# Optimization experiments

Hardware: AMD Instinct MI355X
Metric: run time of the kernel (lower is better)

The kernel has to match this reference:

```python
import jax, jax.numpy as jnp
import numpy as np

N = 100000      # nodes
DEG = 16        # in-degree per node -> E = 1.6M edges
F = 16          # data.x feature dim (19 total - 3 pos dims)
P = 3           # pos dim
H = 64          # hidden_dim
R = 8           # num_regions
C = 8           # num_classes


def _xavier(k, shp):
    lim = np.sqrt(6.0 / (shp[0] + shp[1])).astype(np.float32)
    return jax.random.uniform(k, shp, jnp.float32, -lim, lim)


def setup_inputs() -> dict:
    key = jax.random.key(0)
    ks = jax.random.split(key, 16)
    x = jax.random.normal(ks[0], (N, F), jnp.float32)
    pos = jax.random.uniform(ks[1], (N, P), jnp.float32)
    # every node is a target exactly DEG times so scatter-max is fully covered
    src = jax.random.randint(ks[2], (N * DEG,), 0, N, jnp.int32)
    tgt = jnp.repeat(jnp.arange(N, dtype=jnp.int32), DEG)
    edge_index = jnp.stack([src, tgt])
    # ---- CPU quotient-graph construction (mirrors sklearn KMeans + 3-NN) ----
    pos_np = np.asarray(pos)
    rng = np.random.RandomState(0)
    centers = pos_np[rng.choice(N, R, replace=False)].copy()
    for _ in range(10):  # Lloyd iterations
        d = ((pos_np[:, None, :] - centers[None, :, :]) ** 2).sum(-1)
        labels = d.argmin(1)
        for i in range(R):
            m = labels == i
            if m.any():
                centers[i] = pos_np[m].mean(0)
    cd = ((centers[:, None, :] - centers[None, :, :]) ** 2).sum(-1)
    nn_idx = np.argsort(cd, axis=1)[:, :3]
    conn = []
    for i in range(R):
        for j in nn_idx[i, 1:]:
            conn.append([i, j]); conn.append([j, i])
    quotient_edge_index = jnp.asarray(np.array(conn).T, jnp.int32)
    cluster_labels = jnp.asarray(labels, jnp.int32)
    # ---- parameters (xavier_uniform weights, zero bias) ----
    out = dict(x=x, pos=pos, edge_index=edge_index,
               cluster_labels=cluster_labels,
               quotient_edge_index=quotient_edge_index)
    in_dims = [2 * (F + P), 2 * H, 2 * H, 2 * H]
    for i in range(4):
        out[f"conv{i+1}_W1"] = _xavier(ks[3 + 2 * i], (in_dims[i], H))
        out[f"conv{i+1}_b1"] = jnp.zeros((H,), jnp.float32)
        out[f"conv{i+1}_W2"] = _xavier(ks[4 + 2 * i], (H, H))
        out[f"conv{i+1}_b2"] = jnp.zeros((H,), jnp.float32)
    out["lin_W"] = _xavier(ks[11], (H, C))
    out["lin_b"] = jnp.zeros((C,), jnp.float32)
    return out


def _edge_conv(x, edge_index, W1, b1, W2, b2, num_nodes):
    src, tgt = edge_index[0], edge_index[1]
    x_i = x[tgt]                         # [E, d] target (center)
    x_j = x[src]                         # [E, d] source (neighbor)
    m = jnp.concatenate([x_i, x_j - x_i], axis=1)   # [E, 2d]
    m = jax.nn.relu(m @ W1 + b1) @ W2 + b2          # [E, H]
    agg = jax.ops.segment_max(m, tgt, num_segments=num_nodes)
    # nodes with no incoming edges -> 0 (torch_scatter semantics)
    return jnp.where(jnp.isfinite(agg), agg, 0.0)


def reference(x, pos, edge_index, cluster_labels, quotient_edge_index,
              conv1_W1, conv1_b1, conv1_W2, conv1_b2,
              conv2_W1, conv2_b1, conv2_W2, conv2_b2,
              conv3_W1, conv3_b1, conv3_W2, conv3_b2,
              conv4_W1, conv4_b1, conv4_W2, conv4_b2,
              lin_W, lin_b):
    h = jnp.concatenate([x, pos], axis=1)                       # [N, 19]
    h = jax.nn.relu(_edge_conv(h, edge_index, conv1_W1, conv1_b1, conv1_W2, conv1_b2, N))
    h = jax.nn.relu(_edge_conv(h, edge_index, conv2_W1, conv2_b1, conv2_W2, conv2_b2, N))
    # quotient graph: per-region mean of node features
    sums = jax.ops.segment_sum(h, cluster_labels, num_segments=R)        # [R, H]
    cnt = jax.ops.segment_sum(jnp.ones((h.shape[0], 1), h.dtype), cluster_labels, num_segments=R)
    qx = jnp.where(cnt > 0, sums / jnp.maximum(cnt, 1.0), 0.0)           # [R, H]
    qx = jax.nn.relu(_edge_conv(qx, quotient_edge_index, conv3_W1, conv3_b1, conv3_W2, conv3_b2, R))
    qx = jax.nn.relu(_edge_conv(qx, quotient_edge_index, conv4_W1, conv4_b1, conv4_W2, conv4_b2, R))
    graph_emb = qx.sum(axis=0, keepdims=True)                    # global_add_pool -> [1, H]
    return graph_emb @ lin_W + lin_b                             # [1, C]
```

## Files before the change

### kernel.cpp

```cpp
#include <hip/hip_runtime.h>
#include <hip/hip_fp16.h>

typedef float fv4 __attribute__((ext_vector_type(4)));
using hf8   = __attribute__((ext_vector_type(8))) _Float16;
using f32x4 = __attribute__((ext_vector_type(4))) float;
using u32x4 = __attribute__((ext_vector_type(4))) unsigned;

#define HDIM 64

__device__ __forceinline__ unsigned short f16r(float f) {
    return __half_as_ushort(__float2half(f));
}
__device__ __forceinline__ float hs2f(unsigned short s) {
    return __half2float(__ushort_as_half(s));
}
__device__ __forceinline__ unsigned addrelu2(unsigned ua, unsigned va) {
    unsigned s, r;
    asm("v_pk_add_f16 %0, %1, %2" : "=v"(s) : "v"(ua), "v"(va));
    asm("v_pk_max_f16 %0, %1, 0" : "=v"(r) : "v"(s));
    return r;
}

__global__ void pre1_kernel(
    const float* __restrict__ x, const float* __restrict__ pos,
    const float* __restrict__ W1, const float* __restrict__ b1,
    unsigned short* __restrict__ U, unsigned short* __restrict__ V, int N,
    int mainBlocks,
    const float* __restrict__ W2a, const float* __restrict__ W2b,
    const float* __restrict__ W1c,
    unsigned short* __restrict__ hiA, unsigned short* __restrict__ loA,
    unsigned short* __restrict__ hiB, unsigned short* __restrict__ loB,
    unsigned short* __restrict__ wph, unsigned short* __restrict__ wpl,
    int* __restrict__ qzero)
{
    if ((int)blockIdx.x >= mainBlocks) {
        int idx = (blockIdx.x - mainBlocks) * 256 + threadIdx.x;
        if (idx < 520) qzero[idx] = 0;
        if (idx < 4096) {
            int j = idx >> 6, c = idx & 63;
            float w = W2a[idx];
            unsigned short h = f16r(w);
            unsigned short l = f16r(w - hs2f(h));
            hiA[c * 64 + j] = h; loA[c * 64 + j] = l;
            w = W2b[idx];
            h = f16r(w);
            l = f16r(w - hs2f(h));
            hiB[c * 64 + j] = h; loB[c * 64 + j] = l;
        }
        if (idx < 8192) {
            int d = idx & 63, cp = idx >> 6;
            float w = (cp < 64) ? (W1c[d * 64 + cp] - W1c[(d + 64) * 64 + cp])
                                : W1c[(d + 64) * 64 + (cp - 64)];
            unsigned short h = f16r(w);
            unsigned short l = f16r(w - hs2f(h));
            wph[cp * 64 + d] = h;
            wpl[cp * 64 + d] = l;
        }
        return;
    }

    int lane = threadIdx.x & 63;
    int gw   = (blockIdx.x * blockDim.x + threadIdx.x) >> 6;
    int tw   = (mainBlocks * blockDim.x) >> 6;

    float wd[19], wb[19];
#pragma unroll
    for (int d = 0; d < 19; ++d) {
        float a = W1[d * HDIM + lane];
        float b = W1[(d + 19) * HDIM + lane];
        wd[d] = a - b;
        wb[d] = b;
    }
    float bb = b1[lane];

    for (int n = gw; n < N; n += tw) {
        float su = 0.f, sv = 0.f;
#pragma unroll
        for (int d4 = 0; d4 < 4; ++d4) {
            fv4 h4 = *(const fv4*)&x[(size_t)n * 16 + 4 * d4];
#pragma unroll
            for (int k = 0; k < 4; ++k) {
                su += h4[k] * wd[4 * d4 + k];
                sv += h4[k] * wb[4 * d4 + k];
            }
        }
#pragma unroll
        for (int d = 0; d < 3; ++d) {
            float h = pos[(size_t)n * 3 + d];
            su += h * wd[16 + d];
            sv += h * wb[16 + d];
        }
        U[(size_t)n * HDIM + lane] = f16r(su + bb);
        V[(size_t)n * HDIM + lane] = f16r(sv);
    }
}

__global__ __launch_bounds__(256, 2) void pre_mfma_kernel(
    const unsigned short* __restrict__ h,
    const unsigned short* __restrict__ Whi,
    const unsigned short* __restrict__ Wlo,
    const float* __restrict__ b1,
    unsigned short* __restrict__ U, unsigned short* __restrict__ V, int nTiles)
{
    int lane = threadIdx.x & 63;
    int quad = lane >> 4;
    int m    = lane & 15;
    int gw   = (blockIdx.x * blockDim.x + threadIdx.x) >> 6;
    int tw   = (gridDim.x * blockDim.x) >> 6;

    hf8 Bh[8][2], Bl[8][2];
#pragma unroll
    for (int nt = 0; nt < 8; ++nt)
#pragma unroll
        for (int ks = 0; ks < 2; ++ks) {
            int off = (nt * 16 + m) * 64 + ks * 32 + quad * 8;
            Bh[nt][ks] = *(const hf8*)&Whi[off];
            Bl[nt][ks] = *(const hf8*)&Wlo[off];
        }
    float bias[4];
#pragma unroll
    for (int nt = 0; nt < 4; ++nt) bias[nt] = b1[nt * 16 + m];

    for (int t = gw; t < nTiles; t += tw) {
        int base = t * 16;
        hf8 A[2];
#pragma unroll
        for (int ks = 0; ks < 2; ++ks)
            A[ks] = *(const hf8*)&h[(size_t)(base + m) * HDIM + ks * 32 + quad * 8];

        f32x4 acc[8] = {{0,0,0,0},{0,0,0,0},{0,0,0,0},{0,0,0,0},
                        {0,0,0,0},{0,0,0,0},{0,0,0,0},{0,0,0,0}};
#pragma unroll
        for (int ks = 0; ks < 2; ++ks)
#pragma unroll
            for (int nt = 0; nt < 8; ++nt) {
                acc[nt] = __builtin_amdgcn_mfma_f32_16x16x32_f16(A[ks], Bl[nt][ks], acc[nt], 0, 0, 0);
                acc[nt] = __builtin_amdgcn_mfma_f32_16x16x32_f16(A[ks], Bh[nt][ks], acc[nt], 0, 0, 0);
            }

#pragma unroll
        for (int nt = 0; nt < 8; ++nt) {
            float bv = (nt < 4) ? bias[nt] : 0.f;
            unsigned short* __restrict__ dst = (nt < 4) ? U : V;
            int cc = (nt & 3) * 16 + m;
#pragma unroll
            for (int r = 0; r < 4; ++r) {
                int node = base + quad * 4 + r;
                dst[(size_t)node * HDIM + cc] = f16r(acc[nt][r] + bv);
            }
        }
    }
}

#define FOLD_HALF(V0, V1, OFF)                                                     \
    _Pragma("unroll")                                                              \
    for (int mt = 0; mt < 4; ++mt) {                                               \
        int urow = wave * 8 + (OFF) + mt;                                          \
        u32x4 u0 = *(const u32x4*)((const char*)Ush + urow * 128 + quad * 16);     \
        u32x4 u1 = *(const u32x4*)((const char*)Ush + urow * 128 + 64 + quad * 16);\
        u32x4 a0, a1;                                                              \
        _Pragma("unroll")                                                          \
        for (int p = 0; p < 4; ++p) {                                              \
            a0[p] = addrelu2(u0[p], V0[mt][p]);                                    \
            a1[p] = addrelu2(u1[p], V1[mt][p]);                                    \
        }                                                                          \
        hf8 A0 = __builtin_bit_cast(hf8, a0);                                      \
        hf8 A1 = __builtin_bit_cast(hf8, a1);                                      \
        f32x4 acc[4] = {{0,0,0,0},{0,0,0,0},{0,0,0,0},{0,0,0,0}};                  \
        _Pragma("unroll")                                                          \
        for (int nt = 0; nt < 4; ++nt) {                                           \
            int bb  = nt * 2048 + m * 128 + quad * 16;                             \
            int bs0 = bb ^ ((m & 7) << 4);                                         \
            int bs1 = (bb + 64) ^ ((m & 7) << 4);                                  \
            hf8 Bh0 = *(const hf8*)((const char*)Wsh + bs0);                       \
            hf8 Bl0 = *(const hf8*)((const char*)Wsh + 8192 + bs0);                \
            hf8 Bh1 = *(const hf8*)((const char*)Wsh + bs1);                       \
            hf8 Bl1 = *(const hf8*)((const char*)Wsh + 8192 + bs1);                \
            acc[nt] = __builtin_amdgcn_mfma_f32_16x16x32_f16(A0, Bl0, acc[nt], 0, 0, 0); \
            acc[nt] = __builtin_amdgcn_mfma_f32_16x16x32_f16(A0, Bh0, acc[nt], 0, 0, 0); \
            acc[nt] = __builtin_amdgcn_mfma_f32_16x16x32_f16(A1, Bl1, acc[nt], 0, 0, 0); \
            acc[nt] = __builtin_amdgcn_mfma_f32_16x16x32_f16(A1, Bh1, acc[nt], 0, 0, 0); \
        }                                                                          \
        float mx[4];                                                               \
        _Pragma("unroll")                                                          \
        for (int nt = 0; nt < 4; ++nt)                                             \
            mx[nt] = fmaxf(fmaxf(acc[nt][0], acc[nt][1]), fmaxf(acc[nt][2], acc[nt][3])); \
        _Pragma("unroll")                                                          \
        for (int nt = 0; nt < 4; ++nt) {                                           \
            mx[nt] = fmaxf(mx[nt], __shfl_xor(mx[nt], 16));                        \
            mx[nt] = fmaxf(mx[nt], __shfl_xor(mx[nt], 32));                        \
        }                                                                          \
        float val = (quad == 0) ? mx[0] : (quad == 1) ? mx[1] : (quad == 2) ? mx[2] : mx[3]; \
        out[(size_t)(nb + (OFF) + mt) * HDIM + lane] = f16r(fmaxf(val + b2v, 0.f));\
    }

__global__ __launch_bounds__(256, 3) void edge_mfma_kernel(
    const unsigned short* __restrict__ U, const unsigned short* __restrict__ V,
    const int* __restrict__ src,
    const unsigned short* __restrict__ Whi, const unsigned short* __restrict__ Wlo,
    const float* __restrict__ b2, unsigned short* __restrict__ out)
{
    __shared__ __align__(16) unsigned short Wsh[8192];
    __shared__ __align__(16) unsigned short Ush[2048];

    int tid  = threadIdx.x;
    int wave = tid >> 6;
    int lane = tid & 63;
    int quad = lane >> 4;
    int m    = lane & 15;

    int nbB = blockIdx.x * 32;
    int nb  = nbB + wave * 8;

#pragma unroll
    for (int it = 0; it < 4; ++it) {
        int chunk = it * 256 + tid;
        int reg   = it >> 1;
        int b     = (chunk & 511) * 16;
        int bs    = b ^ (((b >> 7) & 7) << 4);
        const unsigned short* sp = reg ? Wlo : Whi;
        u32x4 d = *(const u32x4*)((const char*)sp + b);
        *(u32x4*)((char*)Wsh + reg * 8192 + bs) = d;
    }
    *(u32x4*)((char*)Ush + tid * 16) =
        *(const u32x4*)((const char*)(U + (size_t)nbB * HDIM) + tid * 16);

    int  srcA = src[(size_t)nb * 16 + lane];
    int  srcB = src[(size_t)(nb + 4) * 16 + lane];
    float b2v = b2[lane];

    __syncthreads();

    u32x4 vA0[4], vA1[4], vB0[4], vB1[4];
#pragma unroll
    for (int mt = 0; mt < 4; ++mt) {
        int s_ = __shfl(srcA, mt * 16 + m);
        const u32x4* vp = (const u32x4*)(V + (size_t)s_ * HDIM + quad * 8);
        vA0[mt] = vp[0]; vA1[mt] = vp[4];
    }
#pragma unroll
    for (int mt = 0; mt < 4; ++mt) {
        int s_ = __shfl(srcB, mt * 16 + m);
        const u32x4* vp = (const u32x4*)(V + (size_t)s_ * HDIM + quad * 8);
        vB0[mt] = vp[0]; vB1[mt] = vp[4];
    }

    FOLD_HALF(vA0, vA1, 0)
    FOLD_HALF(vB0, vB1, 4)
}

__global__ void region_mean_kernel(const unsigned short* __restrict__ h,
                                   const int* __restrict__ labels,
                                   float* __restrict__ qsums, int* __restrict__ qcnt, int N)
{
    __shared__ float ls[8 * 64];
    __shared__ int   lc[8];
    int tid  = threadIdx.x;
    int lane = tid & 63;
    int gw   = (blockIdx.x * blockDim.x + tid) >> 6;
    int tw   = (gridDim.x * blockDim.x) >> 6;

    float acc[8] = {0, 0, 0, 0, 0, 0, 0, 0};
    int   cnt[8] = {0, 0, 0, 0, 0, 0, 0, 0};

    for (int n = gw; n < N; n += tw) {
        int lbl = labels[n];
        float val = hs2f(h[(size_t)n * HDIM + lane]);
#pragma unroll
        for (int r = 0; r < 8; ++r) {
            acc[r] += (lbl == r) ? val : 0.f;
            cnt[r] += (lbl == r) ? 1 : 0;
        }
    }

    if (tid < 8) lc[tid] = 0;
    for (int idx = tid; idx < 512; idx += 256) ls[idx] = 0.f;
    __syncthreads();
#pragma unroll
    for (int r = 0; r < 8; ++r) atomicAdd(&ls[r * 64 + lane], acc[r]);
    if (lane == 0)
#pragma unroll
        for (int r = 0; r < 8; ++r) atomicAdd(&lc[r], cnt[r]);
    __syncthreads();
    for (int idx = tid; idx < 512; idx += 256) atomicAdd(&qsums[idx], ls[idx]);
    if (tid < 8) atomicAdd(&qcnt[tid], lc[tid]);
}

#define EQ_MAX 64
__global__ void tail_kernel(const float* __restrict__ qsums, const int* __restrict__ qcnt,
                            const int* __restrict__ qei, int Eq,
                            const float* __restrict__ W31, const float* __restrict__ b31,
                            const float* __restrict__ W32, const float* __restrict__ b32,
                            const float* __restrict__ W41, const float* __restrict__ b41,
                            const float* __restrict__ W42, const float* __restrict__ b42,
                            const float* __restrict__ linW, const float* __restrict__ linb,
                            float* __restrict__ out)
{
    __shared__ float qx[512], uu[512], vv[512];
    __shared__ float hr[EQ_MAX * 64], me[EQ_MAX * 64];
    __shared__ __align__(16) float W2s[64 * 64];
    __shared__ int   qes[EQ_MAX], qet[EQ_MAX];
    __shared__ float emb[64];

    int tid = threadIdx.x;
    if (Eq > EQ_MAX) Eq = EQ_MAX;

    if (tid < Eq) { qes[tid] = qei[tid]; qet[tid] = qei[Eq + tid]; }
    for (int idx = tid; idx < 512; idx += 256) {
        int r = idx >> 6;
        int cc = qcnt[r];
        qx[idx] = (cc > 0) ? qsums[idx] / (float)cc : 0.f;
    }
    __syncthreads();

    for (int layer = 0; layer < 2; ++layer) {
        const float* W1p = layer ? W41 : W31;
        const float* b1p = layer ? b41 : b31;
        const float* W2p = layer ? W42 : W32;
        const float* b2p = layer ? b42 : b32;

        for (int idx = tid * 4; idx < 4096; idx += 1024)
            *(fv4*)&W2s[idx] = *(const fv4*)&W2p[idx];

        for (int idx = tid; idx < 512; idx += 256) {
            int t = idx >> 6, c = idx & 63;
            float su = 0.f, sv = 0.f;
#pragma unroll 8
            for (int d = 0; d < 64; ++d) {
                float hv = qx[t * 64 + d];
                float a = W1p[d * 64 + c];
                float b = W1p[(d + 64) * 64 + c];
                su += hv * (a - b);
                sv += hv * b;
            }
            uu[idx] = su + b1p[c];
            vv[idx] = sv;
        }
        __syncthreads();

        for (int idx = tid; idx < Eq * 64; idx += 256) {
            int e = idx >> 6, c = idx & 63;
            hr[idx] = fmaxf(uu[qet[e] * 64 + c] + vv[qes[e] * 64 + c], 0.f);
        }
        __syncthreads();

        {
            int c = tid & 63, e0 = tid >> 6;
            for (int e = e0; e < Eq; e += 4) {
                float acc = 0.f;
#pragma unroll 8
                for (int j = 0; j < 64; ++j)
                    acc += hr[e * 64 + j] * W2s[j * 64 + c];
                me[e * 64 + c] = acc;
            }
        }
        __syncthreads();

        for (int idx = tid; idx < 512; idx += 256) {
            int t = idx >> 6, c = idx & 63;
            float a = -INFINITY;
            for (int e = 0; e < Eq; ++e)
                if (qet[e] == t) a = fmaxf(a, me[e * 64 + c]);
            float vout = (a == -INFINITY) ? 0.f : (a + b2p[c]);
            qx[idx] = fmaxf(vout, 0.f);
        }
        __syncthreads();
    }

    if (tid < 64) {
        float s = 0.f;
        for (int r = 0; r < 8; ++r) s += qx[r * 64 + tid];
        emb[tid] = s;
    }
    __syncthreads();
    if (tid < 8) {
        float o = linb[tid];
        for (int c = 0; c < 64; ++c) o += emb[c] * linW[c * 8 + tid];
        out[tid] = o;
    }
}

extern "C" void kernel_launch(void* const* d_in, const int* in_sizes, int n_in,
                              void* d_out, int out_size, void* d_ws, size_t ws_size,
                              hipStream_t stream)
{
    const float* x    = (const float*)d_in[0];
    const float* pos  = (const float*)d_in[1];
    const int*   ei   = (const int*)d_in[2];
    const int*   lbl  = (const int*)d_in[3];
    const int*   qei  = (const int*)d_in[4];
    const float* W11 = (const float*)d_in[5];
    const float* b11 = (const float*)d_in[6];
    const float* W12 = (const float*)d_in[7];
    const float* b12 = (const float*)d_in[8];
    const float* W21 = (const float*)d_in[9];
    const float* b21 = (const float*)d_in[10];
    const float* W22 = (const float*)d_in[11];
    const float* b22 = (const float*)d_in[12];
    const float* W31 = (const float*)d_in[13];
    const float* b31 = (const float*)d_in[14];
    const float* W32 = (const float*)d_in[15];
    const float* b32 = (const float*)d_in[16];
    const float* W41 = (const float*)d_in[17];
    const float* b41 = (const float*)d_in[18];
    const float* W42 = (const float*)d_in[19];
    const float* b42 = (const float*)d_in[20];
    const float* linW = (const float*)d_in[21];
    const float* linb = (const float*)d_in[22];

    int N  = in_sizes[0] / 16;
    int Eq = in_sizes[4] / 2;
    const int* src = ei;

    size_t NH = (size_t)N * HDIM;
    unsigned short* hbf = (unsigned short*)d_ws;
    unsigned short* Ub  = hbf + NH;
    unsigned short* Vb  = Ub + NH;
    unsigned short* w2h1 = Vb + NH;
    unsigned short* w2l1 = w2h1 + 4096;
    unsigned short* w2h2 = w2l1 + 4096;
    unsigned short* w2l2 = w2h2 + 4096;
    unsigned short* wph  = w2l2 + 4096;
    unsigned short* wpl  = wph + 8192;
    float* qsums = (float*)(wpl + 8192);
    int*   qcnt  = (int*)(qsums + 512);

    int nTiles      = N / 16;
    int edgeBlocks  = N / 32;
    int mainBlocks  = 2048;

    pre1_kernel<<<mainBlocks + 32, 256, 0, stream>>>(
        x, pos, W11, b11, Ub, Vb, N, mainBlocks,
        W12, W22, W21, w2h1, w2l1, w2h2, w2l2, wph, wpl, (int*)qsums);
    edge_mfma_kernel<<<edgeBlocks, 256, 0, stream>>>(Ub, Vb, src, w2h1, w2l1, b12, hbf);
    pre_mfma_kernel<<<512, 256, 0, stream>>>(hbf, wph, wpl, b21, Ub, Vb, nTiles);
    edge_mfma_kernel<<<edgeBlocks, 256, 0, stream>>>(Ub, Vb, src, w2h2, w2l2, b22, hbf);
    region_mean_kernel<<<1024, 256, 0, stream>>>(hbf, lbl, qsums, qcnt, N);
    tail_kernel<<<1, 256, 0, stream>>>(qsums, qcnt, qei, Eq,
                                       W31, b31, W32, b32,
                                       W41, b41, W42, b42,
                                       linW, linb, (float*)d_out);
}
```

Baseline: 287.3 us.

## Fuse region-mean pooling into second edge kernel and widen edge tiles

Removes the separate region-mean kernel by accumulating per-label sums in registers inside the second edge-conv kernel, skipping the write of the final node features. Label counts move into pre1's auxiliary blocks and zeroing moves to a memset. The edge kernel now processes 16 nodes per wave with gathers interleaved between folds to overlap latency. The pre-MFMA kernel swaps operands so it can store packed 4-element f16 vectors, and its grid grows. The cost is higher register pressure and larger shared-memory use per block.

```diff
diff --git a/kernel.cpp b/kernel.cpp
--- a/kernel.cpp
+++ b/kernel.cpp
@@ -5,6 +5,7 @@
 using hf8   = __attribute__((ext_vector_type(8))) _Float16;
 using f32x4 = __attribute__((ext_vector_type(4))) float;
 using u32x4 = __attribute__((ext_vector_type(4))) unsigned;
+using u32x2 = __attribute__((ext_vector_type(2))) unsigned;
 
 #define HDIM 64
 
@@ -31,11 +32,10 @@
     unsigned short* __restrict__ hiA, unsigned short* __restrict__ loA,
     unsigned short* __restrict__ hiB, unsigned short* __restrict__ loB,
     unsigned short* __restrict__ wph, unsigned short* __restrict__ wpl,
-    int* __restrict__ qzero)
+    const int* __restrict__ labels, int* __restrict__ qcnt)
 {
     if ((int)blockIdx.x >= mainBlocks) {
         int idx = (blockIdx.x - mainBlocks) * 256 + threadIdx.x;
-        if (idx < 520) qzero[idx] = 0;
         if (idx < 4096) {
             int j = idx >> 6, c = idx & 63;
             float w = W2a[idx];
@@ -55,6 +55,21 @@
             unsigned short l = f16r(w - hs2f(h));
             wph[cp * 64 + d] = h;
             wpl[cp * 64 + d] = l;
+        }
+        {
+            __shared__ int lh[8];
+            int loc[8] = {0, 0, 0, 0, 0, 0, 0, 0};
+            for (int n = idx; n < N; n += 8192) {
+                int l = labels[n];
+#pragma unroll
+                for (int r = 0; r < 8; ++r) loc[r] += (l == r) ? 1 : 0;
+            }
+            if (threadIdx.x < 8) lh[threadIdx.x] = 0;
+            __syncthreads();
+#pragma unroll
+            for (int r = 0; r < 8; ++r) if (loc[r]) atomicAdd(&lh[r], loc[r]);
+            __syncthreads();
+            if (threadIdx.x < 8) atomicAdd(&qcnt[threadIdx.x], lh[threadIdx.x]);
         }
         return;
     }
@@ -117,9 +132,12 @@
             Bh[nt][ks] = *(const hf8*)&Whi[off];
             Bl[nt][ks] = *(const hf8*)&Wlo[off];
         }
-    float bias[4];
-#pragma unroll
-    for (int nt = 0; nt < 4; ++nt) bias[nt] = b1[nt * 16 + m];
+    float bias[16];
+#pragma unroll
+    for (int nt = 0; nt < 4; ++nt)
+#pragma unroll
+        for (int r = 0; r < 4; ++r)
+            bias[nt * 4 + r] = b1[nt * 16 + quad * 4 + r];
 
     for (int t = gw; t < nTiles; t += tw) {
         int base = t * 16;
@@ -134,28 +152,38 @@
         for (int ks = 0; ks < 2; ++ks)
 #pragma unroll
             for (int nt = 0; nt < 8; ++nt) {
-                acc[nt] = __builtin_amdgcn_mfma_f32_16x16x32_f16(A[ks], Bl[nt][ks], acc[nt], 0, 0, 0);
-                acc[nt] = __builtin_amdgcn_mfma_f32_16x16x32_f16(A[ks], Bh[nt][ks], acc[nt], 0, 0, 0);
+                acc[nt] = __builtin_amdgcn_mfma_f32_16x16x32_f16(Bl[nt][ks], A[ks], acc[nt], 0, 0, 0);
+                acc[nt] = __builtin_amdgcn_mfma_f32_16x16x32_f16(Bh[nt][ks], A[ks], acc[nt], 0, 0, 0);
             }
 
 #pragma unroll
         for (int nt = 0; nt < 8; ++nt) {
-            float bv = (nt < 4) ? bias[nt] : 0.f;
             unsigned short* __restrict__ dst = (nt < 4) ? U : V;
-            int cc = (nt & 3) * 16 + m;
-#pragma unroll
-            for (int r = 0; r < 4; ++r) {
-                int node = base + quad * 4 + r;
-                dst[(size_t)node * HDIM + cc] = f16r(acc[nt][r] + bv);
-            }
-        }
-    }
-}
-
-#define FOLD_HALF(V0, V1, OFF)                                                     \
+            int c0 = (nt & 3) * 16 + quad * 4;
+            float a0 = acc[nt][0] + ((nt < 4) ? bias[nt * 4 + 0] : 0.f);
+            float a1 = acc[nt][1] + ((nt < 4) ? bias[nt * 4 + 1] : 0.f);
+            float a2 = acc[nt][2] + ((nt < 4) ? bias[nt * 4 + 2] : 0.f);
+            float a3 = acc[nt][3] + ((nt < 4) ? bias[nt * 4 + 3] : 0.f);
+            u32x2 pk;
+            pk[0] = (unsigned)f16r(a0) | ((unsigned)f16r(a1) << 16);
+            pk[1] = (unsigned)f16r(a2) | ((unsigned)f16r(a3) << 16);
+            *(u32x2*)&dst[(size_t)(base + m) * HDIM + c0] = pk;
+        }
+    }
+}
+
+#define EDGE_ISSUE(SRCR, V0, V1)                                             \
+    _Pragma("unroll")                                                        \
+    for (int mt = 0; mt < 4; ++mt) {                                         \
+        int s_ = __shfl(SRCR, mt * 16 + m);                                  \
+        const u32x4* vp = (const u32x4*)(V + (size_t)s_ * HDIM + quad * 8);  \
+        V0[mt] = vp[0]; V1[mt] = vp[4];                                      \
+    }
+
+#define EDGE_FOLD(V0, V1, OFF)                                                     \
     _Pragma("unroll")                                                              \
     for (int mt = 0; mt < 4; ++mt) {                                               \
-        int urow = wave * 8 + (OFF) + mt;                                          \
+        int urow = wave * 16 + (OFF) + mt;                                         \
         u32x4 u0 = *(const u32x4*)((const char*)Ush + urow * 128 + quad * 16);     \
         u32x4 u1 = *(const u32x4*)((const char*)Ush + urow * 128 + 64 + quad * 16);\
         u32x4 a0, a1;                                                              \
@@ -191,17 +219,26 @@
             mx[nt] = fmaxf(mx[nt], __shfl_xor(mx[nt], 32));                        \
         }                                                                          \
         float val = (quad == 0) ? mx[0] : (quad == 1) ? mx[1] : (quad == 2) ? mx[2] : mx[3]; \
-        out[(size_t)(nb + (OFF) + mt) * HDIM + lane] = f16r(fmaxf(val + b2v, 0.f));\
-    }
-
+        float hv = fmaxf(val + b2v, 0.f);                                          \
+        if constexpr (POOL) {                                                      \
+            int lbl = labels[nb + (OFF) + mt];                                     \
+            _Pragma("unroll")                                                      \
+            for (int r = 0; r < 8; ++r) pacc[r] += (lbl == r) ? hv : 0.f;          \
+        } else {                                                                   \
+            out[(size_t)(nb + (OFF) + mt) * HDIM + lane] = f16r(hv);               \
+        }                                                                          \
+    }
+
+template<int POOL>
 __global__ __launch_bounds__(256, 3) void edge_mfma_kernel(
     const unsigned short* __restrict__ U, const unsigned short* __restrict__ V,
     const int* __restrict__ src,
     const unsigned short* __restrict__ Whi, const unsigned short* __restrict__ Wlo,
-    const float* __restrict__ b2, unsigned short* __restrict__ out)
+    const float* __restrict__ b2, unsigned short* __restrict__ out,
+    const int* __restrict__ labels, float* __restrict__ qsums, int N)
 {
     __shared__ __align__(16) unsigned short Wsh[8192];
-    __shared__ __align__(16) unsigned short Ush[2048];
+    __shared__ __align__(16) unsigned short Ush[4096];
 
     int tid  = threadIdx.x;
     int wave = tid >> 6;
@@ -209,8 +246,9 @@
     int quad = lane >> 4;
     int m    = lane & 15;
 
-    int nbB = blockIdx.x * 32;
-    int nb  = nbB + wave * 8;
+    int nbB = blockIdx.x * 64;
+    int nb  = nbB + wave * 16;
+    bool act = nb < N;
 
 #pragma unroll
     for (int it = 0; it < 4; ++it) {
@@ -222,68 +260,48 @@
         u32x4 d = *(const u32x4*)((const char*)sp + b);
         *(u32x4*)((char*)Wsh + reg * 8192 + bs) = d;
     }
-    *(u32x4*)((char*)Ush + tid * 16) =
-        *(const u32x4*)((const char*)(U + (size_t)nbB * HDIM) + tid * 16);
-
-    int  srcA = src[(size_t)nb * 16 + lane];
-    int  srcB = src[(size_t)(nb + 4) * 16 + lane];
+#pragma unroll
+    for (int it = 0; it < 2; ++it) {
+        int ofs = (it * 256 + tid) * 16;
+        *(u32x4*)((char*)Ush + ofs) =
+            *(const u32x4*)((const char*)(U + (size_t)nbB * HDIM) + ofs);
+    }
+
+    int srcA = 0, srcB = 0, srcC = 0, srcD = 0;
+    if (act) {
+        srcA = src[(size_t)(nb + 0)  * 16 + lane];
+        srcB = src[(size_t)(nb + 4)  * 16 + lane];
+        srcC = src[(size_t)(nb + 8)  * 16 + lane];
+        srcD = src[(size_t)(nb + 12) * 16 + lane];
+    }
     float b2v = b2[lane];
+    float pacc[8] = {0, 0, 0, 0, 0, 0, 0, 0};
 
     __syncthreads();
 
-    u32x4 vA0[4], vA1[4], vB0[4], vB1[4];
-#pragma unroll
-    for (int mt = 0; mt < 4; ++mt) {
-        int s_ = __shfl(srcA, mt * 16 + m);
-        const u32x4* vp = (const u32x4*)(V + (size_t)s_ * HDIM + quad * 8);
-        vA0[mt] = vp[0]; vA1[mt] = vp[4];
-    }
-#pragma unroll
-    for (int mt = 0; mt < 4; ++mt) {
-        int s_ = __shfl(srcB, mt * 16 + m);
-        const u32x4* vp = (const u32x4*)(V + (size_t)s_ * HDIM + quad * 8);
-        vB0[mt] = vp[0]; vB1[mt] = vp[4];
-    }
-
-    FOLD_HALF(vA0, vA1, 0)
-    FOLD_HALF(vB0, vB1, 4)
-}
-
-__global__ void region_mean_kernel(const unsigned short* __restrict__ h,
-                                   const int* __restrict__ labels,
-                                   float* __restrict__ qsums, int* __restrict__ qcnt, int N)
-{
-    __shared__ float ls[8 * 64];
-    __shared__ int   lc[8];
-    int tid  = threadIdx.x;
-    int lane = tid & 63;
-    int gw   = (blockIdx.x * blockDim.x + tid) >> 6;
-    int tw   = (gridDim.x * blockDim.x) >> 6;
-
-    float acc[8] = {0, 0, 0, 0, 0, 0, 0, 0};
-    int   cnt[8] = {0, 0, 0, 0, 0, 0, 0, 0};
-
-    for (int n = gw; n < N; n += tw) {
-        int lbl = labels[n];
-        float val = hs2f(h[(size_t)n * HDIM + lane]);
-#pragma unroll
-        for (int r = 0; r < 8; ++r) {
-            acc[r] += (lbl == r) ? val : 0.f;
-            cnt[r] += (lbl == r) ? 1 : 0;
-        }
-    }
-
-    if (tid < 8) lc[tid] = 0;
-    for (int idx = tid; idx < 512; idx += 256) ls[idx] = 0.f;
-    __syncthreads();
-#pragma unroll
-    for (int r = 0; r < 8; ++r) atomicAdd(&ls[r * 64 + lane], acc[r]);
-    if (lane == 0)
-#pragma unroll
-        for (int r = 0; r < 8; ++r) atomicAdd(&lc[r], cnt[r]);
-    __syncthreads();
-    for (int idx = tid; idx < 512; idx += 256) atomicAdd(&qsums[idx], ls[idx]);
-    if (tid < 8) atomicAdd(&qcnt[tid], lc[tid]);
+    if (act) {
+        u32x4 vA0[4], vA1[4], vB0[4], vB1[4];
+        u32x4 vC0[4], vC1[4], vD0[4], vD1[4];
+        EDGE_ISSUE(srcA, vA0, vA1)
+        EDGE_ISSUE(srcB, vB0, vB1)
+        EDGE_FOLD(vA0, vA1, 0)
+        EDGE_ISSUE(srcC, vC0, vC1)
+        EDGE_FOLD(vB0, vB1, 4)
+        EDGE_ISSUE(srcD, vD0, vD1)
+        EDGE_FOLD(vC0, vC1, 8)
+        EDGE_FOLD(vD0, vD1, 12)
+    }
+
+    if constexpr (POOL) {
+        float* ls = (float*)Ush;
+        __syncthreads();
+        for (int idx = tid; idx < 512; idx += 256) ls[idx] = 0.f;
+        __syncthreads();
+#pragma unroll
+        for (int r = 0; r < 8; ++r) atomicAdd(&ls[r * 64 + lane], pacc[r]);
+        __syncthreads();
+        for (int idx = tid; idx < 512; idx += 256) atomicAdd(&qsums[idx], ls[idx]);
+    }
 }
 
 #define EQ_MAX 64
@@ -425,17 +443,20 @@
     float* qsums = (float*)(wpl + 8192);
     int*   qcnt  = (int*)(qsums + 512);
 
+    (void)hipMemsetAsync(qsums, 0, 512 * sizeof(float) + 8 * sizeof(int), stream);
+
     int nTiles      = N / 16;
-    int edgeBlocks  = N / 32;
+    int edgeBlocks  = (N + 63) / 64;
     int mainBlocks  = 2048;
 
     pre1_kernel<<<mainBlocks + 32, 256, 0, stream>>>(
         x, pos, W11, b11, Ub, Vb, N, mainBlocks,
-        W12, W22, W21, w2h1, w2l1, w2h2, w2l2, wph, wpl, (int*)qsums);
-    edge_mfma_kernel<<<edgeBlocks, 256, 0, stream>>>(Ub, Vb, src, w2h1, w2l1, b12, hbf);
-    pre_mfma_kernel<<<512, 256, 0, stream>>>(hbf, wph, wpl, b21, Ub, Vb, nTiles);
-    edge_mfma_kernel<<<edgeBlocks, 256, 0, stream>>>(Ub, Vb, src, w2h2, w2l2, b22, hbf);
-    region_mean_kernel<<<1024, 256, 0, stream>>>(hbf, lbl, qsums, qcnt, N);
+        W12, W22, W21, w2h1, w2l1, w2h2, w2l2, wph, wpl, lbl, qcnt);
+    edge_mfma_kernel<0><<<edgeBlocks, 256, 0, stream>>>(
+        Ub, Vb, src, w2h1, w2l1, b12, hbf, lbl, qsums, N);
+    pre_mfma_kernel<<<1563, 256, 0, stream>>>(hbf, wph, wpl, b21, Ub, Vb, nTiles);
+    edge_mfma_kernel<1><<<edgeBlocks, 256, 0, stream>>>(
+        Ub, Vb, src, w2h2, w2l2, b22, hbf, lbl, qsums, N);
     tail_kernel<<<1, 256, 0, stream>>>(qsums, qcnt, qei, Eq,
                                        W31, b31, W32, b32,
                                        W41, b41, W42, b42,
```

Measured after the change: 325.1 us. 1.13x slower.
